# Kernel optimization log

Measured on AMD Instinct MI355X. Metric: run time of the kernel, lower is better.

## Reference

```python
import jax, jax.numpy as jnp
import numpy as np

N_NODES = 100000

def setup_inputs() -> dict:
    key = jax.random.key(0)
    k1, k2, k3, k4, k5 = jax.random.split(key, 5)
    feature = jax.random.normal(k1, (N_NODES, 64), dtype=jnp.float32)
    src = jax.random.randint(k2, (1600000,), 0, N_NODES, dtype=jnp.int64)
    dst = jax.random.randint(k3, (1600000,), 0, N_NODES, dtype=jnp.int64)
    W = jax.random.normal(k4, (64, 128), dtype=jnp.float32) * 0.05  # nn.Linear(128, 64).weight
    b = jax.random.normal(k5, (64,), dtype=jnp.float32) * 0.05
    return {"feature": feature, "src": src, "dst": dst, "W": W, "b": b}

def reference(feature, src, dst, W, b):
    # copy_src + sum: for each edge, message = feature[src]; sum into dst node
    agg = jax.ops.segment_sum(feature[src], dst, num_segments=feature.shape[0])  # [N, d]
    h = jnp.concatenate([feature, agg], axis=1)  # [N, 2d]
    return h @ W.T + b  # Linear(2d -> out)
```

## Files before the change

### kernel.cpp

```cpp
#include <hip/hip_runtime.h>

#define DFEAT 64
#define BKSZ 512
#define SB 9
#define NBKT_PAD 256
#define PLACE_CHUNK 4096
#define FILL_CAP 12288

typedef __attribute__((ext_vector_type(8))) short bf16x8;
typedef __attribute__((ext_vector_type(4))) float f32x4;

__device__ inline unsigned short f2bf(float f) {
  unsigned int x = __float_as_uint(f);
  return (unsigned short)((x + 0x7fffu + ((x >> 16) & 1u)) >> 16);
}

__global__ __launch_bounds__(256) void gcn_prep(
    const float4* __restrict__ feat4, ushort4* __restrict__ gb4, int n4,
    const float4* __restrict__ w4, ushort4* __restrict__ wb4, int nw4,
    const int* __restrict__ dst, int* __restrict__ bcnt,
    int n_edges, int nbkt) {
  int total = n4 + 16 + nw4;
  for (int i = blockIdx.x * 256 + threadIdx.x; i < total; i += gridDim.x * 256) {
    if (i < n4) {
      float4 f = feat4[i];
      ushort4 u;
      u.x = f2bf(f.x); u.y = f2bf(f.y); u.z = f2bf(f.z); u.w = f2bf(f.w);
      gb4[i] = u;
    } else if (i < n4 + 16) {
      gb4[i] = (ushort4){0, 0, 0, 0};
    } else {
      float4 f = w4[i - n4 - 16];
      ushort4 u;
      u.x = f2bf(f.x); u.y = f2bf(f.y); u.z = f2bf(f.z); u.w = f2bf(f.w);
      wb4[i - n4 - 16] = u;
    }
  }
  __shared__ int h[NBKT_PAD];
  for (int i = threadIdx.x; i < nbkt; i += 256) h[i] = 0;
  __syncthreads();
  int ne4 = n_edges >> 2;
  const int4* d4 = (const int4*)dst;
  for (int e = blockIdx.x * 256 + threadIdx.x; e < ne4; e += gridDim.x * 256) {
    int4 v = d4[e];
    atomicAdd(&h[v.x >> SB], 1);
    atomicAdd(&h[v.y >> SB], 1);
    atomicAdd(&h[v.z >> SB], 1);
    atomicAdd(&h[v.w >> SB], 1);
  }
  if (blockIdx.x == 0)
    for (int e = (ne4 << 2) + threadIdx.x; e < n_edges; e += 256)
      atomicAdd(&h[dst[e] >> SB], 1);
  __syncthreads();
  for (int i = threadIdx.x; i < nbkt; i += 256)
    if (h[i]) atomicAdd(&bcnt[i], h[i]);
}

__global__ __launch_bounds__(512) void gcn_place(
    const int* __restrict__ src, const int* __restrict__ dst,
    const int* __restrict__ bcnt, int* __restrict__ bcur,
    unsigned int* __restrict__ pairs, int n_edges, int nbkt) {
  __shared__ int sc[2][NBKT_PAD];
  __shared__ int cnt[NBKT_PAD];
  __shared__ int base[NBKT_PAD];
  __shared__ unsigned int pk[PLACE_CHUNK];
  __shared__ unsigned char bk[PLACE_CHUNK];
  int t = threadIdx.x;

  if (t < NBKT_PAD) sc[0][t] = (t < nbkt) ? bcnt[t] : 0;
  __syncthreads();
  int pin = 0;
  for (int s = 1; s < NBKT_PAD; s <<= 1) {
    int po = pin ^ 1;
    if (t < NBKT_PAD) {
      int v = sc[pin][t];
      if (t >= s) v += sc[pin][t - s];
      sc[po][t] = v;
    }
    __syncthreads();
    pin = po;
  }
  int bb = 0;
  if (t < NBKT_PAD) bb = (t == 0) ? 0 : sc[pin][t - 1];
  if (t < NBKT_PAD) cnt[t] = 0;
  __syncthreads();

  int e0 = blockIdx.x * PLACE_CHUNK;
  int e1 = min(e0 + PLACE_CHUNK, n_edges);
  for (int e = e0 + t; e < e1; e += 512) {
    int d = dst[e];
    int s = src[e];
    int b = d >> SB;
    pk[e - e0] = (unsigned)s | ((unsigned)(d & (BKSZ - 1)) << 23);
    bk[e - e0] = (unsigned char)b;
    atomicAdd(&cnt[b], 1);
  }
  __syncthreads();
  if (t < NBKT_PAD) {
    int c = cnt[t];
    base[t] = bb + (c ? atomicAdd(&bcur[t], c) : 0);
    cnt[t] = 0;
  }
  __syncthreads();
  for (int e = e0 + t; e < e1; e += 512) {
    int b = bk[e - e0];
    int pos = base[b] + atomicAdd(&cnt[b], 1);
    pairs[pos] = pk[e - e0];
  }
}

__global__ __launch_bounds__(512) void gcn_fillk(
    const unsigned int* __restrict__ pairs, const int* __restrict__ bcnt,
    int* __restrict__ offsets, int* __restrict__ edge_src,
    int n_nodes, int n_edges, int nbkt) {
  __shared__ int sc[2][NBKT_PAD];
  __shared__ int deg[BKSZ];
  __shared__ int buf[2][BKSZ];
  __shared__ int cur[BKSZ];
  __shared__ unsigned int lp[FILL_CAP];
  int b = blockIdx.x, t = threadIdx.x;

  if (t < NBKT_PAD) sc[0][t] = (t < nbkt) ? bcnt[t] : 0;
  __syncthreads();
  int pin = 0;
  for (int s = 1; s < NBKT_PAD; s <<= 1) {
    int po = pin ^ 1;
    if (t < NBKT_PAD) {
      int v = sc[pin][t];
      if (t >= s) v += sc[pin][t - s];
      sc[po][t] = v;
    }
    __syncthreads();
    pin = po;
  }
  int e0 = (b == 0) ? 0 : sc[pin][b - 1];
  int e1 = sc[pin][b];
  int ne = e1 - e0;
  int n0 = b << SB;
  bool fits = (ne <= FILL_CAP);

  deg[t] = 0;
  __syncthreads();
  if (fits) {
    for (int i = t; i < ne; i += 512) {
      unsigned p = pairs[e0 + i];
      lp[i] = p;
      atomicAdd(&deg[p >> 23], 1);
    }
  } else {
    for (int i = t; i < ne; i += 512) atomicAdd(&deg[pairs[e0 + i] >> 23], 1);
  }
  __syncthreads();
  buf[0][t] = deg[t];
  __syncthreads();
  pin = 0;
  for (int s = 1; s < BKSZ; s <<= 1) {
    int po = pin ^ 1;
    int v = buf[pin][t];
    if (t >= s) v += buf[pin][t - s];
    buf[po][t] = v;
    __syncthreads();
    pin = po;
  }
  int excl = (t == 0) ? 0 : buf[pin][t - 1];
  cur[t] = excl;
  int n = n0 + t;
  if (n < n_nodes) offsets[n] = e0 + excl;
  if (b == nbkt - 1 && t == 0) offsets[n_nodes] = n_edges;
  __syncthreads();
  if (fits) {
    for (int i = t; i < ne; i += 512) {
      unsigned p = lp[i];
      int pos = atomicAdd(&cur[p >> 23], 1);
      edge_src[e0 + pos] = (int)(p & 0x7FFFFFu);
    }
  } else {
    for (int i = t; i < ne; i += 512) {
      unsigned p = pairs[e0 + i];
      int pos = atomicAdd(&cur[p >> 23], 1);
      edge_src[e0 + pos] = (int)(p & 0x7FFFFFu);
    }
  }
}

__global__ __launch_bounds__(128, 8) void gcn_gather_mfma(
    const ushort4* __restrict__ gb4,
    const unsigned short* __restrict__ wb,
    const int* __restrict__ edge_src,
    const int* __restrict__ offsets,
    const float* __restrict__ bias,
    float* __restrict__ out,
    int n_nodes) {
  __shared__ unsigned short hl[2][16 * 64];
  int tid = threadIdx.x;
  int wave = tid >> 6, lane = tid & 63;
  int q = lane >> 4, kk = lane & 15;
  int lrow = lane & 15, lkg = lane >> 4;
  unsigned short* myhl = hl[wave];
  int node0 = blockIdx.x * 32 + wave * 16;
  const int SENT = n_nodes;

  int oidx = node0 + ((lane < 16) ? lane : 16);
  if (oidx > n_nodes) oidx = n_nodes;
  int offv = offsets[oidx];
  int nvalid = n_nodes - node0;
  if (nvalid > 16) nvalid = 16;

  int idv = SENT;
  if (nvalid > 0) {
    int o0 = __shfl(offv, 0);
    int d0 = __shfl(offv, 1) - o0;
    if (lane < d0) idv = edge_src[o0 + lane];
  }

  for (int r = 0; r < nvalid; ++r) {
    int off = __shfl(offv, r);
    int deg = __shfl(offv, r + 1) - off;

    int idnx = SENT;
    if (r + 1 < nvalid) {
      int o2 = __shfl(offv, r + 1);
      int d2 = __shfl(offv, r + 2) - o2;
      if (lane < d2) idnx = edge_src[o2 + lane];
    }

    float4 a0 = {0.f, 0.f, 0.f, 0.f}, a1 = a0, a2 = a0, a3 = a0;
    auto proc16 = [&](int idreg, int j) {
      int s0 = __shfl(idreg, j + q);
      int s1 = __shfl(idreg, j + 4 + q);
      int s2 = __shfl(idreg, j + 8 + q);
      int s3 = __shfl(idreg, j + 12 + q);
      uint2 w0 = *(const uint2*)&gb4[s0 * 16 + kk];
      uint2 w1 = *(const uint2*)&gb4[s1 * 16 + kk];
      uint2 w2 = *(const uint2*)&gb4[s2 * 16 + kk];
      uint2 w3 = *(const uint2*)&gb4[s3 * 16 + kk];
      a0.x += __uint_as_float(w0.x << 16);
      a0.y += __uint_as_float(w0.x & 0xffff0000u);
      a0.z += __uint_as_float(w0.y << 16);
      a0.w += __uint_as_float(w0.y & 0xffff0000u);
      a1.x += __uint_as_float(w1.x << 16);
      a1.y += __uint_as_float(w1.x & 0xffff0000u);
      a1.z += __uint_as_float(w1.y << 16);
      a1.w += __uint_as_float(w1.y & 0xffff0000u);
      a2.x += __uint_as_float(w2.x << 16);
      a2.y += __uint_as_float(w2.x & 0xffff0000u);
      a2.z += __uint_as_float(w2.y << 16);
      a2.w += __uint_as_float(w2.y & 0xffff0000u);
      a3.x += __uint_as_float(w3.x << 16);
      a3.y += __uint_as_float(w3.x & 0xffff0000u);
      a3.z += __uint_as_float(w3.y << 16);
      a3.w += __uint_as_float(w3.y & 0xffff0000u);
    };

    int lim = min(deg, 64);
    for (int j = 0; j < lim; j += 16) proc16(idv, j);
    for (int base = 64; base < deg; base += 64) {
      int id2 = (base + lane < deg) ? edge_src[off + base + lane] : SENT;
      int lim2 = min(64, deg - base);
      for (int j = 0; j < lim2; j += 16) proc16(id2, j);
    }

    float4 acc;
    acc.x = (a0.x + a1.x) + (a2.x + a3.x);
    acc.y = (a0.y + a1.y) + (a2.y + a3.y);
    acc.z = (a0.z + a1.z) + (a2.z + a3.z);
    acc.w = (a0.w + a1.w) + (a2.w + a3.w);
    acc.x += __shfl_xor(acc.x, 16); acc.x += __shfl_xor(acc.x, 32);
    acc.y += __shfl_xor(acc.y, 16); acc.y += __shfl_xor(acc.y, 32);
    acc.z += __shfl_xor(acc.z, 16); acc.z += __shfl_xor(acc.z, 32);
    acc.w += __shfl_xor(acc.w, 16); acc.w += __shfl_xor(acc.w, 32);

    if (q == 0) {
      unsigned swz = (unsigned)((r & 7) << 4);
      char* rowp = (char*)(myhl + r * 64);
      ushort4 pk;
      pk.x = f2bf(acc.x); pk.y = f2bf(acc.y);
      pk.z = f2bf(acc.z); pk.w = f2bf(acc.w);
      *(ushort4*)(rowp + ((8u * (unsigned)kk) ^ swz)) = pk;
    }
    idv = idnx;
  }

  bf16x8 wf[4][4];
#pragma unroll
  for (int kt = 0; kt < 4; ++kt)
#pragma unroll
    for (int jt = 0; jt < 4; ++jt)
      wf[kt][jt] =
          *(const bf16x8*)(wb + (jt * 16 + lrow) * 128 + kt * 32 + lkg * 8);

  f32x4 acc[4];
#pragma unroll
  for (int jt = 0; jt < 4; ++jt) acc[jt] = (f32x4){0.f, 0.f, 0.f, 0.f};

  int nrow = node0 + lrow;
  int nload = (nrow < n_nodes) ? nrow : n_nodes;
#pragma unroll
  for (int kt = 0; kt < 2; ++kt) {
    bf16x8 af = *(const bf16x8*)((const unsigned short*)gb4 +
                                 (size_t)nload * DFEAT + kt * 32 + lkg * 8);
#pragma unroll
    for (int jt = 0; jt < 4; ++jt)
      acc[jt] = __builtin_amdgcn_mfma_f32_16x16x32_bf16(af, wf[kt][jt],
                                                        acc[jt], 0, 0, 0);
  }
  unsigned aswz = (unsigned)((lrow & 7) << 4);
  const char* arow = (const char*)(myhl + lrow * 64);
#pragma unroll
  for (int kt = 2; kt < 4; ++kt) {
    bf16x8 af =
        *(const bf16x8*)(arow + ((unsigned)((kt - 2) * 64 + lkg * 16) ^ aswz));
#pragma unroll
    for (int jt = 0; jt < 4; ++jt)
      acc[jt] = __builtin_amdgcn_mfma_f32_16x16x32_bf16(af, wf[kt][jt],
                                                        acc[jt], 0, 0, 0);
  }

#pragma unroll
  for (int jt = 0; jt < 4; ++jt) {
    float bj = bias[jt * 16 + lrow];
#pragma unroll
    for (int r = 0; r < 4; ++r) {
      int n = node0 + lkg * 4 + r;
      if (n < n_nodes) out[n * DFEAT + jt * 16 + lrow] = acc[jt][r] + bj;
    }
  }
}

__global__ __launch_bounds__(256) void gcn_scatter_kernel(
    const float4* __restrict__ feat4, const int* __restrict__ src,
    const int* __restrict__ dst, float* __restrict__ agg, int n_edges) {
  long long gid = (long long)blockIdx.x * blockDim.x + threadIdx.x;
  int e = (int)(gid >> 4);
  int c = (int)(gid & 15);
  if (e >= n_edges) return;
  float4 v = feat4[src[e] * 16 + c];
  float* p = agg + dst[e] * DFEAT + c * 4;
  atomicAdd(p + 0, v.x);
  atomicAdd(p + 1, v.y);
  atomicAdd(p + 2, v.z);
  atomicAdd(p + 3, v.w);
}

__global__ __launch_bounds__(256) void gcn_gemm_kernel(
    const float* __restrict__ feat, const float* __restrict__ agg,
    const float* __restrict__ W, const float* __restrict__ bias,
    float* __restrict__ out, int n_nodes) {
  __shared__ float4 Wl4[2048];
  __shared__ __align__(16) float hlf[16][128];
  int tid = threadIdx.x;
  for (int i = tid; i < 2048; i += 256) {
    int j = i >> 5, k4 = i & 31;
    Wl4[k4 * 64 + (j ^ (k4 & 7))] = ((const float4*)W)[i];
  }
  int node0 = blockIdx.x * 16;
  int wave = tid >> 6, lane = tid & 63;
  int mbase = wave * 4;
#pragma unroll
  for (int r = 0; r < 4; ++r) {
    int n = node0 + mbase + r;
    if (n < n_nodes) {
      hlf[mbase + r][lane]      = feat[n * DFEAT + lane];
      hlf[mbase + r][64 + lane] = agg[n * DFEAT + lane];
    }
  }
  __syncthreads();
  float a0 = 0.f, a1 = 0.f, a2 = 0.f, a3 = 0.f;
#pragma unroll 4
  for (int k4 = 0; k4 < 32; ++k4) {
    float4 w  = Wl4[k4 * 64 + (lane ^ (k4 & 7))];
    float4 h0 = *((const float4*)&hlf[mbase + 0][k4 * 4]);
    float4 h1 = *((const float4*)&hlf[mbase + 1][k4 * 4]);
    float4 h2 = *((const float4*)&hlf[mbase + 2][k4 * 4]);
    float4 h3 = *((const float4*)&hlf[mbase + 3][k4 * 4]);
    a0 += w.x * h0.x + w.y * h0.y + w.z * h0.z + w.w * h0.w;
    a1 += w.x * h1.x + w.y * h1.y + w.z * h1.z + w.w * h1.w;
    a2 += w.x * h2.x + w.y * h2.y + w.z * h2.z + w.w * h2.w;
    a3 += w.x * h3.x + w.y * h3.y + w.z * h3.z + w.w * h3.w;
  }
  float bj = bias[lane];
  int n = node0 + mbase;
  if (n + 0 < n_nodes) out[(n + 0) * DFEAT + lane] = a0 + bj;
  if (n + 1 < n_nodes) out[(n + 1) * DFEAT + lane] = a1 + bj;
  if (n + 2 < n_nodes) out[(n + 2) * DFEAT + lane] = a2 + bj;
  if (n + 3 < n_nodes) out[(n + 3) * DFEAT + lane] = a3 + bj;
}


extern "C" void kernel_launch(void* const* d_in, const int* in_sizes, int n_in,
                              void* d_out, int out_size, void* d_ws, size_t ws_size,
                              hipStream_t stream) {
  const float* feat = (const float*)d_in[0];
  const int*   src  = (const int*)d_in[1];
  const int*   dst  = (const int*)d_in[2];
  const float* W    = (const float*)d_in[3];
  const float* bias = (const float*)d_in[4];
  float* out = (float*)d_out;

  int n_nodes = in_sizes[0] / DFEAT;
  int n_edges = in_sizes[1];
  int nbkt = (n_nodes + BKSZ - 1) >> SB;

  auto align_up = [](size_t x) { return (x + 255) & ~(size_t)255; };
  size_t esrc_b = align_up((size_t)n_edges * 4);
  size_t off_b  = align_up((size_t)(n_nodes + 1) * 4);
  size_t bcnt_b = align_up((size_t)NBKT_PAD * 4);
  size_t bcur_b = align_up((size_t)NBKT_PAD * 4);
  size_t wb_b   = align_up((size_t)DFEAT * 128 * 2);
  size_t gb_b   = align_up((size_t)(n_nodes + 1) * DFEAT * 2);
  size_t need   = esrc_b + off_b + bcnt_b + bcur_b + wb_b + gb_b;

  bool pairs_fit = (size_t)out_size * 4 >= (size_t)n_edges * 4;
  bool ok = pairs_fit && nbkt >= 1 && nbkt <= NBKT_PAD && ws_size >= need &&
            n_nodes < (1 << 23);

  if (ok) {
    char* p = (char*)d_ws;
    int* edge_src = (int*)p;   p += esrc_b;
    int* offsets  = (int*)p;   p += off_b;
    int* bcnt     = (int*)p;   p += bcnt_b;
    int* bcur     = (int*)p;   p += bcur_b;
    unsigned short* wb = (unsigned short*)p;   p += wb_b;
    unsigned short* gb = (unsigned short*)p;
    unsigned int* pairs = (unsigned int*)d_out;

    hipMemsetAsync(bcnt, 0, bcnt_b + bcur_b, stream);

    int n4 = n_nodes * (DFEAT / 4);
    int nw4 = DFEAT * 128 / 4;
    gcn_prep<<<1024, 256, 0, stream>>>(
        (const float4*)feat, (ushort4*)gb, n4,
        (const float4*)W, (ushort4*)wb, nw4,
        dst, bcnt, n_edges, nbkt);

    int pblocks = (n_edges + PLACE_CHUNK - 1) / PLACE_CHUNK;
    gcn_place<<<pblocks, 512, 0, stream>>>(src, dst, bcnt, bcur, pairs,
                                           n_edges, nbkt);

    gcn_fillk<<<nbkt, 512, 0, stream>>>(pairs, bcnt, offsets, edge_src,
                                        n_nodes, n_edges, nbkt);

    int gblocks = (n_nodes + 31) / 32;
    gcn_gather_mfma<<<gblocks, 128, 0, stream>>>(
        (const ushort4*)gb, wb, edge_src, offsets, bias, out, n_nodes);
  } else {
    size_t agg_bytes = (size_t)n_nodes * DFEAT * sizeof(float);
    float* agg = (ws_size >= agg_bytes) ? (float*)d_ws : out;
    hipMemsetAsync(agg, 0, agg_bytes, stream);
    long long st = (long long)n_edges * 16;
    gcn_scatter_kernel<<<(int)((st + 255) / 256), 256, 0, stream>>>(
        (const float4*)feat, src, dst, agg, n_edges);
    int gblocks = (n_nodes + 15) / 16;
    gcn_gemm_kernel<<<gblocks, 256, 0, stream>>>(feat, agg, W, bias, out,
                                                 n_nodes);
  }
}
```

Before: 118.4 us.

## Drop bucket histogram pass using fixed-capacity bucket slots with overflow list

Removes the separate destination histogram pass. Each bucket now gets a fixed-capacity region (CAP entries) in the pairs buffer, so edges can be placed without first knowing the global prefix sums. Edges beyond a bucket's capacity go to a global overflow list that the fill kernel scans. Feature and weight conversion is merged into the place kernel, which removes one launch and one full read of dst. The cost is a larger pairs footprint and a scan of the whole overflow list by every fill block.

```diff
diff --git a/kernel.cpp b/kernel.cpp
--- a/kernel.cpp
+++ b/kernel.cpp
@@ -5,6 +5,7 @@
 #define SB 9
 #define NBKT_PAD 256
 #define PLACE_CHUNK 4096
+#define CAP 12288
 #define FILL_CAP 12288
 
 typedef __attribute__((ext_vector_type(8))) short bf16x8;
@@ -15,13 +16,15 @@
   return (unsigned short)((x + 0x7fffu + ((x >> 16) & 1u)) >> 16);
 }
 
-__global__ __launch_bounds__(256) void gcn_prep(
+__global__ __launch_bounds__(512) void gcn_place_conv(
     const float4* __restrict__ feat4, ushort4* __restrict__ gb4, int n4,
     const float4* __restrict__ w4, ushort4* __restrict__ wb4, int nw4,
-    const int* __restrict__ dst, int* __restrict__ bcnt,
+    const int* __restrict__ src, const int* __restrict__ dst,
+    int* __restrict__ bcur, int* __restrict__ ocnt,
+    unsigned int* __restrict__ pairs, int2* __restrict__ ov,
     int n_edges, int nbkt) {
   int total = n4 + 16 + nw4;
-  for (int i = blockIdx.x * 256 + threadIdx.x; i < total; i += gridDim.x * 256) {
+  for (int i = blockIdx.x * 512 + threadIdx.x; i < total; i += gridDim.x * 512) {
     if (i < n4) {
       float4 f = feat4[i];
       ushort4 u;
@@ -36,52 +39,12 @@
       wb4[i - n4 - 16] = u;
     }
   }
-  __shared__ int h[NBKT_PAD];
-  for (int i = threadIdx.x; i < nbkt; i += 256) h[i] = 0;
-  __syncthreads();
-  int ne4 = n_edges >> 2;
-  const int4* d4 = (const int4*)dst;
-  for (int e = blockIdx.x * 256 + threadIdx.x; e < ne4; e += gridDim.x * 256) {
-    int4 v = d4[e];
-    atomicAdd(&h[v.x >> SB], 1);
-    atomicAdd(&h[v.y >> SB], 1);
-    atomicAdd(&h[v.z >> SB], 1);
-    atomicAdd(&h[v.w >> SB], 1);
-  }
-  if (blockIdx.x == 0)
-    for (int e = (ne4 << 2) + threadIdx.x; e < n_edges; e += 256)
-      atomicAdd(&h[dst[e] >> SB], 1);
-  __syncthreads();
-  for (int i = threadIdx.x; i < nbkt; i += 256)
-    if (h[i]) atomicAdd(&bcnt[i], h[i]);
-}
-
-__global__ __launch_bounds__(512) void gcn_place(
-    const int* __restrict__ src, const int* __restrict__ dst,
-    const int* __restrict__ bcnt, int* __restrict__ bcur,
-    unsigned int* __restrict__ pairs, int n_edges, int nbkt) {
-  __shared__ int sc[2][NBKT_PAD];
+
   __shared__ int cnt[NBKT_PAD];
   __shared__ int base[NBKT_PAD];
   __shared__ unsigned int pk[PLACE_CHUNK];
   __shared__ unsigned char bk[PLACE_CHUNK];
   int t = threadIdx.x;
-
-  if (t < NBKT_PAD) sc[0][t] = (t < nbkt) ? bcnt[t] : 0;
-  __syncthreads();
-  int pin = 0;
-  for (int s = 1; s < NBKT_PAD; s <<= 1) {
-    int po = pin ^ 1;
-    if (t < NBKT_PAD) {
-      int v = sc[pin][t];
-      if (t >= s) v += sc[pin][t - s];
-      sc[po][t] = v;
-    }
-    __syncthreads();
-    pin = po;
-  }
-  int bb = 0;
-  if (t < NBKT_PAD) bb = (t == 0) ? 0 : sc[pin][t - 1];
   if (t < NBKT_PAD) cnt[t] = 0;
   __syncthreads();
 
@@ -98,29 +61,44 @@
   __syncthreads();
   if (t < NBKT_PAD) {
     int c = cnt[t];
-    base[t] = bb + (c ? atomicAdd(&bcur[t], c) : 0);
+    base[t] = c ? atomicAdd(&bcur[t], c) : 0;
     cnt[t] = 0;
   }
   __syncthreads();
   for (int e = e0 + t; e < e1; e += 512) {
     int b = bk[e - e0];
-    int pos = base[b] + atomicAdd(&cnt[b], 1);
-    pairs[pos] = pk[e - e0];
+    int rel = base[b] + atomicAdd(&cnt[b], 1);
+    unsigned p = pk[e - e0];
+    if (rel < CAP) {
+      pairs[b * CAP + rel] = p;
+    } else {
+      int oi = atomicAdd(ocnt, 1);
+      ov[oi] = make_int2((int)(p & 0x7FFFFFu), (b << 9) | (int)(p >> 23));
+    }
   }
 }
 
 __global__ __launch_bounds__(512) void gcn_fillk(
-    const unsigned int* __restrict__ pairs, const int* __restrict__ bcnt,
+    const unsigned int* __restrict__ pairs, const int2* __restrict__ ov,
+    const int* __restrict__ ocnt_p, const int* __restrict__ bcur,
     int* __restrict__ offsets, int* __restrict__ edge_src,
     int n_nodes, int n_edges, int nbkt) {
   __shared__ int sc[2][NBKT_PAD];
+  __shared__ int ovb[NBKT_PAD];
   __shared__ int deg[BKSZ];
   __shared__ int buf[2][BKSZ];
   __shared__ int cur[BKSZ];
   __shared__ unsigned int lp[FILL_CAP];
   int b = blockIdx.x, t = threadIdx.x;
-
-  if (t < NBKT_PAD) sc[0][t] = (t < nbkt) ? bcnt[t] : 0;
+  int onum = ocnt_p[0];
+
+  if (t < NBKT_PAD) ovb[t] = 0;
+  __syncthreads();
+  for (int i = t; i < onum; i += 512) atomicAdd(&ovb[ov[i].y >> 9], 1);
+  __syncthreads();
+
+  if (t < NBKT_PAD)
+    sc[0][t] = (t < nbkt) ? (min(bcur[t], CAP) + ovb[t]) : 0;
   __syncthreads();
   int pin = 0;
   for (int s = 1; s < NBKT_PAD; s <<= 1) {
@@ -134,21 +112,25 @@
     pin = po;
   }
   int e0 = (b == 0) ? 0 : sc[pin][b - 1];
-  int e1 = sc[pin][b];
-  int ne = e1 - e0;
+  int mc = min(bcur[b], CAP);
   int n0 = b << SB;
-  bool fits = (ne <= FILL_CAP);
+  bool fits = (mc <= FILL_CAP);
 
   deg[t] = 0;
   __syncthreads();
   if (fits) {
-    for (int i = t; i < ne; i += 512) {
-      unsigned p = pairs[e0 + i];
+    for (int i = t; i < mc; i += 512) {
+      unsigned p = pairs[b * CAP + i];
       lp[i] = p;
       atomicAdd(&deg[p >> 23], 1);
     }
   } else {
-    for (int i = t; i < ne; i += 512) atomicAdd(&deg[pairs[e0 + i] >> 23], 1);
+    for (int i = t; i < mc; i += 512)
+      atomicAdd(&deg[pairs[b * CAP + i] >> 23], 1);
+  }
+  for (int i = t; i < onum; i += 512) {
+    int2 o = ov[i];
+    if ((o.y >> 9) == b) atomicAdd(&deg[o.y & (BKSZ - 1)], 1);
   }
   __syncthreads();
   buf[0][t] = deg[t];
@@ -169,16 +151,23 @@
   if (b == nbkt - 1 && t == 0) offsets[n_nodes] = n_edges;
   __syncthreads();
   if (fits) {
-    for (int i = t; i < ne; i += 512) {
+    for (int i = t; i < mc; i += 512) {
       unsigned p = lp[i];
       int pos = atomicAdd(&cur[p >> 23], 1);
       edge_src[e0 + pos] = (int)(p & 0x7FFFFFu);
     }
   } else {
-    for (int i = t; i < ne; i += 512) {
-      unsigned p = pairs[e0 + i];
+    for (int i = t; i < mc; i += 512) {
+      unsigned p = pairs[b * CAP + i];
       int pos = atomicAdd(&cur[p >> 23], 1);
       edge_src[e0 + pos] = (int)(p & 0x7FFFFFu);
+    }
+  }
+  for (int i = t; i < onum; i += 512) {
+    int2 o = ov[i];
+    if ((o.y >> 9) == b) {
+      int pos = atomicAdd(&cur[o.y & (BKSZ - 1)], 1);
+      edge_src[e0 + pos] = o.x;
     }
   }
 }
@@ -404,13 +393,14 @@
   auto align_up = [](size_t x) { return (x + 255) & ~(size_t)255; };
   size_t esrc_b = align_up((size_t)n_edges * 4);
   size_t off_b  = align_up((size_t)(n_nodes + 1) * 4);
-  size_t bcnt_b = align_up((size_t)NBKT_PAD * 4);
   size_t bcur_b = align_up((size_t)NBKT_PAD * 4);
+  size_t ocnt_b = align_up(4);
   size_t wb_b   = align_up((size_t)DFEAT * 128 * 2);
   size_t gb_b   = align_up((size_t)(n_nodes + 1) * DFEAT * 2);
-  size_t need   = esrc_b + off_b + bcnt_b + bcur_b + wb_b + gb_b;
-
-  bool pairs_fit = (size_t)out_size * 4 >= (size_t)n_edges * 4;
+  size_t need   = esrc_b + off_b + bcur_b + ocnt_b + wb_b + gb_b;
+
+  size_t ov_need = (n_edges > CAP) ? (size_t)(n_edges - CAP) * 8 : 0;
+  bool pairs_fit = (size_t)out_size * 4 >= (size_t)nbkt * CAP * 4 + ov_need;
   bool ok = pairs_fit && nbkt >= 1 && nbkt <= NBKT_PAD && ws_size >= need &&
             n_nodes < (1 << 23);
 
@@ -418,27 +408,25 @@
     char* p = (char*)d_ws;
     int* edge_src = (int*)p;   p += esrc_b;
     int* offsets  = (int*)p;   p += off_b;
-    int* bcnt     = (int*)p;   p += bcnt_b;
     int* bcur     = (int*)p;   p += bcur_b;
+    int* ocnt     = (int*)p;   p += ocnt_b;
     unsigned short* wb = (unsigned short*)p;   p += wb_b;
     unsigned short* gb = (unsigned short*)p;
     unsigned int* pairs = (unsigned int*)d_out;
-
-    hipMemsetAsync(bcnt, 0, bcnt_b + bcur_b, stream);
+    int2* ov = (int2*)((char*)d_out + (size_t)nbkt * CAP * 4);
+
+    hipMemsetAsync(bcur, 0, bcur_b + ocnt_b, stream);
 
     int n4 = n_nodes * (DFEAT / 4);
     int nw4 = DFEAT * 128 / 4;
-    gcn_prep<<<1024, 256, 0, stream>>>(
+    int pblocks = (n_edges + PLACE_CHUNK - 1) / PLACE_CHUNK;
+    gcn_place_conv<<<pblocks, 512, 0, stream>>>(
         (const float4*)feat, (ushort4*)gb, n4,
         (const float4*)W, (ushort4*)wb, nw4,
-        dst, bcnt, n_edges, nbkt);
-
-    int pblocks = (n_edges + PLACE_CHUNK - 1) / PLACE_CHUNK;
-    gcn_place<<<pblocks, 512, 0, stream>>>(src, dst, bcnt, bcur, pairs,
-                                           n_edges, nbkt);
-
-    gcn_fillk<<<nbkt, 512, 0, stream>>>(pairs, bcnt, offsets, edge_src,
-                                        n_nodes, n_edges, nbkt);
+        src, dst, bcur, ocnt, pairs, ov, n_edges, nbkt);
+
+    gcn_fillk<<<nbkt, 512, 0, stream>>>(pairs, ov, ocnt, bcur, offsets,
+                                        edge_src, n_nodes, n_edges, nbkt);
 
     int gblocks = (n_nodes + 31) / 32;
     gcn_gather_mfma<<<gblocks, 128, 0, stream>>>(
```

Measured after the change: 94.87 us (median of 2 runs). -19.8%, faster.
